# Performance work log

Hardware: AMD Instinct MI355X
Metric: run time of the kernel (lower is better)

Reference implementation:

```python
import jax, jax.numpy as jnp
import numpy as np

B, N, M = 4, 50000, 256
BIN_MIN, BIN_MAX = -3.0, 3.0


def setup_inputs() -> dict:
    key = jax.random.key(0)
    kx, ky = jax.random.split(key)
    x_coords = jax.random.normal(kx, (B, N), dtype=jnp.float32)
    y_coords = jax.random.normal(ky, (B, N), dtype=jnp.float32)
    bins = jnp.linspace(BIN_MIN, BIN_MAX, M, dtype=jnp.float32)
    return {"x_coords": x_coords, "y_coords": y_coords, "bins": bins}


def reference(x_coords, y_coords, bins):
    # bandwidth defaults to bin resolution (bins[1] - bins[0])
    bandwidth = bins[1] - bins[0]
    # per-axis Gaussian kernel values: (B, N, M)
    kx = jnp.exp(-0.5 * jnp.square((x_coords[..., None] - bins) / bandwidth))
    ky = jnp.exp(-0.5 * jnp.square((y_coords[..., None] - bins) / bandwidth))
    # joint kernel values reduced over particles: (B, M, M)
    joint = jnp.einsum("bni,bnj->bij", kx, ky)
    norm = jnp.sum(joint, axis=(-2, -1), keepdims=True) + 1e-10
    return joint / norm
```

## Files before the change

kernel.cpp:

```cpp
#include <hip/hip_runtime.h>


#define B_     4
#define N_     50000
#define M_     256
#define BK     64
#define NCH    48
#define KSTEPS 17
#define KCH    (KSTEPS * BK)
#define LDKB   80
#define ROWS   129
#define AXB    (ROWS * LDKB)
#define BUFB   (2 * AXB)
#define BLOCK  256
#define WINB   7
#define CS2    0.72134752f
#define L127   6.9886847f

#if __has_builtin(__builtin_amdgcn_exp2f)
  #define EXP2(t) __builtin_amdgcn_exp2f(t)
#else
  #define EXP2(t) exp2f(t)
#endif

typedef __attribute__((ext_vector_type(4))) int i32x4;

__device__ __forceinline__ unsigned short bf16ru(float f) {
    return (unsigned short)((__builtin_bit_cast(unsigned, f) + 0x8000u) >> 16);
}
__device__ __forceinline__ float bf2f(unsigned short u) {
    return __builtin_bit_cast(float, ((unsigned)u) << 16);
}

__global__ __launch_bounds__(BLOCK) void kde_gemm(
    const float* __restrict__ xs, const float* __restrict__ ys,
    const float* __restrict__ bins, unsigned short* __restrict__ partial,
    float* __restrict__ ws2, int wide)
{
    __shared__ __align__(16) char tiles[2][2][ROWS][LDKB];
    __shared__ float sred[4];

    const int tid   = threadIdx.x;
    const int tile  = blockIdx.x;
    const int chunk = blockIdx.y;
    const int b     = blockIdx.z;

    const int ilo = (tile & 1) * 128;
    const int jlo = (tile >> 1) * 128;
    const float bin0  = bins[0];
    const float invbw = 1.0f / (bins[1] - bin0);

    {
        int4* za = (int4*)&tiles[0][0][0][0];
        const int4 z4 = {0, 0, 0, 0};
        for (int t = tid; t < (int)(sizeof(tiles) / 16); t += BLOCK) za[t] = z4;
    }

    const int  h       = tid & 1;
    const int  jn      = 4 - h;
    const int  jbase   = h << 2;
    const int  kcol    = (tid >> 1) & 63;
    const int  axis    = (tid >> 7) & 1;
    const int  rowlo   = axis ? jlo : ilo;
    const int  colbase = axis * AXB + kcol;
    const float* coord = (axis ? ys : xs) + b * N_;
    const int  k0 = chunk * KCH;
    char* const tb = &tiles[0][0][0][0];

    const int w    = tid >> 6;
    const int R0   = (w >> 1) * 64;
    const int wj   = (w & 1) * 64;
    const int lane = tid & 63;
    const int lm   = lane & 15;
    const int quad = lane >> 4;
    unsigned short* pb = partial + (((size_t)chunk * B_ + b) << 16);

    i32x4 acc[4][4];
    #pragma unroll
    for (int mt = 0; mt < 4; ++mt)
        #pragma unroll
        for (int nt = 0; nt < 4; ++nt) acc[mt][nt] = i32x4{0, 0, 0, 0};

    int ps0 = 1 << 20, ps1 = 1 << 20;

    float v0 = 3.0e30f, vnext = 3.0e30f;
    {
        const int ka = k0 + kcol;       if (ka  < N_) v0    = coord[ka];
        const int kb2 = k0 + BK + kcol; if (kb2 < N_) vnext = coord[kb2];
    }
    __syncthreads();

    {
        const float u  = (v0 - bin0) * invbw;
        const float st = rintf(u) - 3.0f;
        const float d0 = u - st;
        const int rr0 = (int)st - rowlo;
        ps0 = rr0;
        const int dmp = colbase + 128 * LDKB;
        #pragma unroll
        for (int j = 0; j < 4; ++j) {
            if (j < jn) {
                const int jj = jbase + j;
                const float d = d0 - (float)jj;
                const float E = EXP2(fmaf(-CS2 * d, d, L127));
                const int rr = rr0 + jj;
                tb[((unsigned)rr < 128u) ? (colbase + rr * LDKB) : dmp] =
                    (char)(int)(E + 0.5f);
            }
        }
    }
    __syncthreads();

    for (int ks = 0; ks < KSTEPS; ++ks) {
        const int q = ks & 1;
        float vpre = 3.0e30f;
        if ((ks + 2) < KSTEPS) {
            const int ka = k0 + (ks + 2) * BK + kcol;
            if (ka < N_) vpre = coord[ka];
        }
        if ((ks + 1) < KSTEPS) {
            const int qn  = q ^ 1;
            const int bqn = qn * BUFB + colbase;
            const int dmp = bqn + 128 * LDKB;
            const int ps  = qn ? ps1 : ps0;
            if (ps < (1 << 19)) {
                #pragma unroll
                for (int j = 0; j < 4; ++j) {
                    if (j < jn) {
                        const int rr = ps + jbase + j;
                        tb[((unsigned)rr < 128u) ? (bqn + rr * LDKB) : dmp] = 0;
                    }
                }
            }
            const float u  = (vnext - bin0) * invbw;
            const float st = rintf(u) - 3.0f;
            const float d0 = u - st;
            const int rr0 = (int)st - rowlo;
            if (qn) ps1 = rr0; else ps0 = rr0;
            #pragma unroll
            for (int j = 0; j < 4; ++j) {
                if (j < jn) {
                    const int jj = jbase + j;
                    const float d = d0 - (float)jj;
                    const float E = EXP2(fmaf(-CS2 * d, d, L127));
                    const int rr = rr0 + jj;
                    tb[((unsigned)rr < 128u) ? (bqn + rr * LDKB) : dmp] =
                        (char)(int)(E + 0.5f);
                }
            }
        }
        vnext = vpre;

        const char* bufA = tb + q * BUFB;
        const char* bufB = tb + q * BUFB + AXB;
        i32x4 af[4], bfr[4];
        #pragma unroll
        for (int t4 = 0; t4 < 4; ++t4)
            af[t4] = *(const i32x4*)(bufA + (R0 + t4 * 16 + lm) * LDKB + quad * 16);
        #pragma unroll
        for (int t4 = 0; t4 < 4; ++t4)
            bfr[t4] = *(const i32x4*)(bufB + (wj + t4 * 16 + lm) * LDKB + quad * 16);
        #pragma unroll
        for (int mt = 0; mt < 4; ++mt)
            #pragma unroll
            for (int nt = 0; nt < 4; ++nt)
                acc[mt][nt] = __builtin_amdgcn_mfma_i32_16x16x64_i8(
                    af[mt], bfr[nt], acc[mt][nt], 0, 0, 0);
        __syncthreads();
    }

    float tsum = 0.f;
    #pragma unroll
    for (int mt = 0; mt < 4; ++mt) {
        const int row0 = ilo + R0 + mt * 16 + quad * 4;
        #pragma unroll
        for (int nt = 0; nt < 4; ++nt) {
            const int col = jlo + wj + nt * 16 + lm;
            const i32x4 a = acc[mt][nt];
            #pragma unroll
            for (int e = 0; e < 4; ++e) {
                const float v = (float)a[e];
                pb[(size_t)(row0 + e) * M_ + col] = bf16ru(v);
                tsum += v;
            }
        }
    }

    #pragma unroll
    for (int off = 32; off; off >>= 1) tsum += __shfl_xor(tsum, off);
    if (lane == 0) sred[w] = tsum;
    __syncthreads();
    if (tid == 0) {
        const float bsum = sred[0] + sred[1] + sred[2] + sred[3];
        if (wide) {
            const int bid = (b * NCH + chunk) * 4 + tile;
            ws2[bid] = bsum;
        } else {
            atomicAdd(&ws2[b], bsum);
        }
    }
}

__global__ __launch_bounds__(BLOCK) void kde_tail(
    const unsigned short* __restrict__ partial, const float* __restrict__ ws2,
    float* __restrict__ out, int wide)
{
    __shared__ float sred[4];
    __shared__ float snorm;
    const int tid = threadIdx.x;
    const int cellIdx = blockIdx.x * BLOCK + tid;
    const int bb = cellIdx >> 14;
    const int cb = cellIdx & 16383;

    float nrm;
    if (wide) {
        float t = (tid < 4 * NCH) ? ws2[bb * 4 * NCH + tid] : 0.f;
        #pragma unroll
        for (int off = 32; off; off >>= 1) t += __shfl_xor(t, off);
        if ((tid & 63) == 0) sred[tid >> 6] = t;
        __syncthreads();
        if (tid == 0) snorm = sred[0] + sred[1] + sred[2] + sred[3];
        __syncthreads();
        nrm = snorm;
    } else {
        nrm = ws2[bb];
    }

    float4 a = {0.f, 0.f, 0.f, 0.f};
    #pragma unroll 4
    for (int c = 0; c < NCH; ++c) {
        const ushort4 v = *(const ushort4*)(partial +
            (((size_t)c * B_ + bb) << 16) + (size_t)cb * 4);
        a.x += bf2f(v.x); a.y += bf2f(v.y); a.z += bf2f(v.z); a.w += bf2f(v.w);
    }
    const float sc = 1.0f / (nrm + 1e-10f);
    a.x *= sc; a.y *= sc; a.z *= sc; a.w *= sc;
    ((float4*)out)[cellIdx] = a;
}

extern "C" void kernel_launch(void* const* d_in, const int* in_sizes, int n_in,
                              void* d_out, int out_size, void* d_ws, size_t ws_size,
                              hipStream_t stream)
{
    const float* xs   = (const float*)d_in[0];
    const float* ys   = (const float*)d_in[1];
    const float* bins = (const float*)d_in[2];
    float* out = (float*)d_out;
    unsigned short* partial = (unsigned short*)d_ws;
    const size_t PSZ = (size_t)NCH * B_ * M_ * M_ * sizeof(unsigned short);
    float* ws2 = (float*)((char*)d_ws + PSZ);

    const int wide = (ws_size >= PSZ + 4096) ? 1 : 0;
    if (!wide) hipMemsetAsync(ws2, 0, 4 * sizeof(float), stream);

    kde_gemm<<<dim3(4, NCH, B_), dim3(BLOCK), 0, stream>>>(
        xs, ys, bins, partial, ws2, wide);
    kde_tail<<<dim3(B_ * M_ * M_ / (4 * BLOCK)), dim3(BLOCK), 0, stream>>>(
        partial, ws2, out, wide);
}
```

Baseline: 88.16 us.

## Pre-bucket particles per output tile so GEMM skips non-contributing particles

```diff
diff --git a/kernel.cpp b/kernel.cpp
--- a/kernel.cpp
+++ b/kernel.cpp
@@ -6,14 +6,12 @@
 #define M_     256
 #define BK     64
 #define NCH    48
-#define KSTEPS 17
-#define KCH    (KSTEPS * BK)
 #define LDKB   80
 #define ROWS   129
 #define AXB    (ROWS * LDKB)
 #define BUFB   (2 * AXB)
 #define BLOCK  256
-#define WINB   7
+#define CAP    65536
 #define CS2    0.72134752f
 #define L127   6.9886847f
 
@@ -32,10 +30,112 @@
     return __builtin_bit_cast(float, ((unsigned)u) << 16);
 }
 
+__global__ __launch_bounds__(BLOCK) void kde_bucket(
+    const float* __restrict__ xs, const float* __restrict__ ys,
+    const float* __restrict__ bins, int4* __restrict__ lists,
+    int* __restrict__ counts)
+{
+    const int b = blockIdx.y;
+    const int k = blockIdx.x * BLOCK + threadIdx.x;
+    const float bin0  = bins[0];
+    const float invbw = 1.0f / (bins[1] - bin0);
+    const bool valid = (k < N_);
+
+    const float x = valid ? xs[b * N_ + k] : 3.0e30f;
+    const float y = valid ? ys[b * N_ + k] : 3.0e30f;
+    const float ux = (x - bin0) * invbw;
+    const float uy = (y - bin0) * invbw;
+    const float stx = rintf(ux) - 3.0f;
+    const float sty = rintf(uy) - 3.0f;
+    const float dx0 = ux - stx;
+    const float dy0 = uy - sty;
+    const int rx = (int)stx;
+    const int ry = (int)sty;
+
+    unsigned qx[7], qy[7];
+    #pragma unroll
+    for (int j = 0; j < 7; ++j) {
+        const float dx = dx0 - (float)j;
+        const float dy = dy0 - (float)j;
+        qx[j] = (unsigned)(int)(EXP2(fmaf(-CS2 * dx, dx, L127)) + 0.5f) & 255u;
+        qy[j] = (unsigned)(int)(EXP2(fmaf(-CS2 * dy, dy, L127)) + 0.5f) & 255u;
+    }
+
+    const bool mx[2] = { valid && rx >= -6  && rx <= 127,
+                         valid && rx >= 122 && rx <= 255 };
+    const bool my[2] = { valid && ry >= -6  && ry <= 127,
+                         valid && ry >= 122 && ry <= 255 };
+
+    const int lane = threadIdx.x & 63;
+    #pragma unroll
+    for (int ti = 0; ti < 2; ++ti) {
+        #pragma unroll
+        for (int tj = 0; tj < 2; ++tj) {
+            const bool m = mx[ti] && my[tj];
+            const unsigned long long mask = __ballot(m);
+            if (mask) {
+                const int li = (b * 2 + ti) * 2 + tj;
+                const int leader = __ffsll((unsigned long long)mask) - 1;
+                int base = 0;
+                if (lane == leader)
+                    base = atomicAdd(&counts[li], __popcll(mask));
+                base = __shfl(base, leader);
+                if (m) {
+                    const int off =
+                        __popcll(mask & ((1ull << lane) - 1ull));
+                    const unsigned rxl = (unsigned)(rx - ti * 128 + 8) & 255u;
+                    const unsigned ryl = (unsigned)(ry - tj * 128 + 8) & 255u;
+                    int4 e;
+                    e.x = (int)(rxl | (ryl << 8) | (qx[0] << 16) | (qx[1] << 24));
+                    e.y = (int)(qx[2] | (qx[3] << 8) | (qx[4] << 16) | (qx[5] << 24));
+                    e.z = (int)(qx[6] | (qy[0] << 8) | (qy[1] << 16) | (qy[2] << 24));
+                    e.w = (int)(qy[3] | (qy[4] << 8) | (qy[5] << 16) | (qy[6] << 24));
+                    lists[(size_t)li * CAP + base + off] = e;
+                }
+            }
+        }
+    }
+}
+
+__device__ __forceinline__ void scat(char* __restrict__ tb, const int4 e,
+                                     const int axis, const int h,
+                                     const int cbq, int& ps)
+{
+    const int jbase = h << 2;
+    const int dmp = cbq + 128 * LDKB;
+    if (ps < (1 << 19)) {
+        const int pr = ps + jbase;
+        tb[((unsigned)(pr    ) < 128u) ? (cbq + (pr    ) * LDKB) : dmp] = 0;
+        tb[((unsigned)(pr + 1) < 128u) ? (cbq + (pr + 1) * LDKB) : dmp] = 0;
+        tb[((unsigned)(pr + 2) < 128u) ? (cbq + (pr + 2) * LDKB) : dmp] = 0;
+        if (!h)
+            tb[((unsigned)(pr + 3) < 128u) ? (cbq + (pr + 3) * LDKB) : dmp] = 0;
+    }
+    const int rl = ((axis ? (e.x >> 8) : e.x) & 255) - 8;
+    int q0, q1, q2, q3;
+    if (axis == 0) {
+        q0 = h ? ((e.y >> 16) & 255) : ((e.x >> 16) & 255);
+        q1 = h ? (int)((unsigned)e.y >> 24) : (int)((unsigned)e.x >> 24);
+        q2 = h ? (e.z & 255) : (e.y & 255);
+        q3 = (e.y >> 8) & 255;
+    } else {
+        q0 = h ? ((e.w >> 8) & 255) : ((e.z >> 8) & 255);
+        q1 = h ? ((e.w >> 16) & 255) : ((e.z >> 16) & 255);
+        q2 = h ? (int)((unsigned)e.w >> 24) : (int)((unsigned)e.z >> 24);
+        q3 = e.w & 255;
+    }
+    ps = rl;
+    const int rr = rl + jbase;
+    tb[((unsigned)(rr    ) < 128u) ? (cbq + (rr    ) * LDKB) : dmp] = (char)q0;
+    tb[((unsigned)(rr + 1) < 128u) ? (cbq + (rr + 1) * LDKB) : dmp] = (char)q1;
+    tb[((unsigned)(rr + 2) < 128u) ? (cbq + (rr + 2) * LDKB) : dmp] = (char)q2;
+    if (!h)
+        tb[((unsigned)(rr + 3) < 128u) ? (cbq + (rr + 3) * LDKB) : dmp] = (char)q3;
+}
+
 __global__ __launch_bounds__(BLOCK) void kde_gemm(
-    const float* __restrict__ xs, const float* __restrict__ ys,
-    const float* __restrict__ bins, unsigned short* __restrict__ partial,
-    float* __restrict__ ws2, int wide)
+    const int4* __restrict__ lists, const int* __restrict__ counts,
+    unsigned short* __restrict__ partial, float* __restrict__ ws2, int wide)
 {
     __shared__ __align__(16) char tiles[2][2][ROWS][LDKB];
     __shared__ float sred[4];
@@ -45,10 +145,20 @@
     const int chunk = blockIdx.y;
     const int b     = blockIdx.z;
 
-    const int ilo = (tile & 1) * 128;
-    const int jlo = (tile >> 1) * 128;
-    const float bin0  = bins[0];
-    const float invbw = 1.0f / (bins[1] - bin0);
+    const int ti  = tile & 1;
+    const int tj  = tile >> 1;
+    const int ilo = ti * 128;
+    const int jlo = tj * 128;
+
+    const int li  = (b * 2 + ti) * 2 + tj;
+    const int len = counts[li];
+    const int seg = (len + NCH - 1) / NCH;
+    const int start = chunk * seg;
+    int myn = len - start;
+    if (myn < 0) myn = 0;
+    if (myn > seg) myn = seg;
+    const int ksteps = (myn + 63) >> 6;
+    const int4* lst = lists + (size_t)li * CAP + start;
 
     {
         int4* za = (int4*)&tiles[0][0][0][0];
@@ -56,15 +166,10 @@
         for (int t = tid; t < (int)(sizeof(tiles) / 16); t += BLOCK) za[t] = z4;
     }
 
-    const int  h       = tid & 1;
-    const int  jn      = 4 - h;
-    const int  jbase   = h << 2;
-    const int  kcol    = (tid >> 1) & 63;
-    const int  axis    = (tid >> 7) & 1;
-    const int  rowlo   = axis ? jlo : ilo;
-    const int  colbase = axis * AXB + kcol;
-    const float* coord = (axis ? ys : xs) + b * N_;
-    const int  k0 = chunk * KCH;
+    const int h     = tid & 1;
+    const int kcol  = (tid >> 1) & 63;
+    const int axis  = (tid >> 7) & 1;
+    const int colbase = axis * AXB + kcol;
     char* const tb = &tiles[0][0][0][0];
 
     const int w    = tid >> 6;
@@ -83,73 +188,27 @@
 
     int ps0 = 1 << 20, ps1 = 1 << 20;
 
-    float v0 = 3.0e30f, vnext = 3.0e30f;
-    {
-        const int ka = k0 + kcol;       if (ka  < N_) v0    = coord[ka];
-        const int kb2 = k0 + BK + kcol; if (kb2 < N_) vnext = coord[kb2];
-    }
+    const int4 DUM = {0x0000FFFF, 0, 0, 0};
+    int4 e0 = DUM, enext = DUM;
+    if (kcol < myn)      e0    = lst[kcol];
+    if (BK + kcol < myn) enext = lst[BK + kcol];
+
     __syncthreads();
 
-    {
-        const float u  = (v0 - bin0) * invbw;
-        const float st = rintf(u) - 3.0f;
-        const float d0 = u - st;
-        const int rr0 = (int)st - rowlo;
-        ps0 = rr0;
-        const int dmp = colbase + 128 * LDKB;
-        #pragma unroll
-        for (int j = 0; j < 4; ++j) {
-            if (j < jn) {
-                const int jj = jbase + j;
-                const float d = d0 - (float)jj;
-                const float E = EXP2(fmaf(-CS2 * d, d, L127));
-                const int rr = rr0 + jj;
-                tb[((unsigned)rr < 128u) ? (colbase + rr * LDKB) : dmp] =
-                    (char)(int)(E + 0.5f);
-            }
+    if (ksteps > 0)
+        scat(tb, e0, axis, h, colbase, ps0);
+    __syncthreads();
+
+    for (int ks = 0; ks < ksteps; ++ks) {
+        const int q = ks & 1;
+        int4 epre = DUM;
+        const int ka = (ks + 2) * BK + kcol;
+        if ((ks + 2) < ksteps && ka < myn) epre = lst[ka];
+        if ((ks + 1) < ksteps) {
+            if (q) scat(tb, enext, axis, h, colbase, ps0);
+            else   scat(tb, enext, axis, h, BUFB + colbase, ps1);
         }
-    }
-    __syncthreads();
-
-    for (int ks = 0; ks < KSTEPS; ++ks) {
-        const int q = ks & 1;
-        float vpre = 3.0e30f;
-        if ((ks + 2) < KSTEPS) {
-            const int ka = k0 + (ks + 2) * BK + kcol;
-            if (ka < N_) vpre = coord[ka];
-        }
-        if ((ks + 1) < KSTEPS) {
-            const int qn  = q ^ 1;
-            const int bqn = qn * BUFB + colbase;
-            const int dmp = bqn + 128 * LDKB;
-            const int ps  = qn ? ps1 : ps0;
-            if (ps < (1 << 19)) {
-                #pragma unroll
-                for (int j = 0; j < 4; ++j) {
-                    if (j < jn) {
-                        const int rr = ps + jbase + j;
-                        tb[((unsigned)rr < 128u) ? (bqn + rr * LDKB) : dmp] = 0;
-                    }
-                }
-            }
-            const float u  = (vnext - bin0) * invbw;
-            const float st = rintf(u) - 3.0f;
-            const float d0 = u - st;
-            const int rr0 = (int)st - rowlo;
-            if (qn) ps1 = rr0; else ps0 = rr0;
-            #pragma unroll
-            for (int j = 0; j < 4; ++j) {
-                if (j < jn) {
-                    const int jj = jbase + j;
-                    const float d = d0 - (float)jj;
-                    const float E = EXP2(fmaf(-CS2 * d, d, L127));
-                    const int rr = rr0 + jj;
-                    tb[((unsigned)rr < 128u) ? (bqn + rr * LDKB) : dmp] =
-                        (char)(int)(E + 0.5f);
-                }
-            }
-        }
-        vnext = vpre;
+        enext = epre;
 
         const char* bufA = tb + q * BUFB;
         const char* bufB = tb + q * BUFB + AXB;
@@ -246,15 +305,21 @@
     const float* ys   = (const float*)d_in[1];
     const float* bins = (const float*)d_in[2];
     float* out = (float*)d_out;
+
     unsigned short* partial = (unsigned short*)d_ws;
     const size_t PSZ = (size_t)NCH * B_ * M_ * M_ * sizeof(unsigned short);
-    float* ws2 = (float*)((char*)d_ws + PSZ);
+    float* ws2   = (float*)((char*)d_ws + PSZ);
+    int*   counts = (int*)((char*)d_ws + PSZ + 4096);
+    int4*  lists  = (int4*)((char*)d_ws + PSZ + 8192);
 
     const int wide = (ws_size >= PSZ + 4096) ? 1 : 0;
     if (!wide) hipMemsetAsync(ws2, 0, 4 * sizeof(float), stream);
-
+    hipMemsetAsync(counts, 0, 16 * sizeof(int), stream);
+
+    kde_bucket<<<dim3((N_ + BLOCK - 1) / BLOCK, B_), dim3(BLOCK), 0, stream>>>(
+        xs, ys, bins, lists, counts);
     kde_gemm<<<dim3(4, NCH, B_), dim3(BLOCK), 0, stream>>>(
-        xs, ys, bins, partial, ws2, wide);
+        lists, counts, partial, ws2, wide);
     kde_tail<<<dim3(B_ * M_ * M_ / (4 * BLOCK)), dim3(BLOCK), 0, stream>>>(
         partial, ws2, out, wide);
 }
```

Measured after the change: 226.2 us. +156.6%, slower.

## Replace int8 MFMA outer-product GEMM with LDS atomic scatter of 7x7 stencils

Applied to the files above, without the earlier changes.

```diff
diff --git a/kernel.cpp b/kernel.cpp
--- a/kernel.cpp
+++ b/kernel.cpp
@@ -4,16 +4,13 @@
 #define B_     4
 #define N_     50000
 #define M_     256
-#define BK     64
-#define NCH    48
-#define KSTEPS 17
-#define KCH    (KSTEPS * BK)
-#define LDKB   80
-#define ROWS   129
-#define AXB    (ROWS * LDKB)
-#define BUFB   (2 * AXB)
+#define NCH    32
+#define NST    2
+#define CHUNK  ((N_ + NCH - 1) / NCH)
 #define BLOCK  256
-#define WINB   7
+#define GROWS  128
+#define GCELLS (GROWS * M_)
+#define GSZ    33088
 #define CS2    0.72134752f
 #define L127   6.9886847f
 
@@ -23,8 +20,6 @@
   #define EXP2(t) exp2f(t)
 #endif
 
-typedef __attribute__((ext_vector_type(4))) int i32x4;
-
 __device__ __forceinline__ unsigned short bf16ru(float f) {
     return (unsigned short)((__builtin_bit_cast(unsigned, f) + 0x8000u) >> 16);
 }
@@ -32,158 +27,98 @@
     return __builtin_bit_cast(float, ((unsigned)u) << 16);
 }
 
-__global__ __launch_bounds__(BLOCK) void kde_gemm(
+__global__ __launch_bounds__(BLOCK) void kde_accum(
     const float* __restrict__ xs, const float* __restrict__ ys,
     const float* __restrict__ bins, unsigned short* __restrict__ partial,
     float* __restrict__ ws2, int wide)
 {
-    __shared__ __align__(16) char tiles[2][2][ROWS][LDKB];
+    __shared__ __align__(16) unsigned int G[GSZ];
     __shared__ float sred[4];
 
     const int tid   = threadIdx.x;
-    const int tile  = blockIdx.x;
+    const int strip = blockIdx.x;
     const int chunk = blockIdx.y;
     const int b     = blockIdx.z;
+    const int lane  = tid & 63;
+    const int w     = tid >> 6;
 
-    const int ilo = (tile & 1) * 128;
-    const int jlo = (tile >> 1) * 128;
     const float bin0  = bins[0];
     const float invbw = 1.0f / (bins[1] - bin0);
+    const int   rlo   = strip * GROWS;
 
     {
-        int4* za = (int4*)&tiles[0][0][0][0];
-        const int4 z4 = {0, 0, 0, 0};
-        for (int t = tid; t < (int)(sizeof(tiles) / 16); t += BLOCK) za[t] = z4;
-    }
-
-    const int  h       = tid & 1;
-    const int  jn      = 4 - h;
-    const int  jbase   = h << 2;
-    const int  kcol    = (tid >> 1) & 63;
-    const int  axis    = (tid >> 7) & 1;
-    const int  rowlo   = axis ? jlo : ilo;
-    const int  colbase = axis * AXB + kcol;
-    const float* coord = (axis ? ys : xs) + b * N_;
-    const int  k0 = chunk * KCH;
-    char* const tb = &tiles[0][0][0][0];
-
-    const int w    = tid >> 6;
-    const int R0   = (w >> 1) * 64;
-    const int wj   = (w & 1) * 64;
-    const int lane = tid & 63;
-    const int lm   = lane & 15;
-    const int quad = lane >> 4;
-    unsigned short* pb = partial + (((size_t)chunk * B_ + b) << 16);
-
-    i32x4 acc[4][4];
-    #pragma unroll
-    for (int mt = 0; mt < 4; ++mt)
-        #pragma unroll
-        for (int nt = 0; nt < 4; ++nt) acc[mt][nt] = i32x4{0, 0, 0, 0};
-
-    int ps0 = 1 << 20, ps1 = 1 << 20;
-
-    float v0 = 3.0e30f, vnext = 3.0e30f;
-    {
-        const int ka = k0 + kcol;       if (ka  < N_) v0    = coord[ka];
-        const int kb2 = k0 + BK + kcol; if (kb2 < N_) vnext = coord[kb2];
+        uint4* gz = (uint4*)G;
+        const uint4 z4 = {0u, 0u, 0u, 0u};
+        for (int t = tid; t < GSZ / 4; t += BLOCK) gz[t] = z4;
     }
     __syncthreads();
 
-    {
-        const float u  = (v0 - bin0) * invbw;
-        const float st = rintf(u) - 3.0f;
-        const float d0 = u - st;
-        const int rr0 = (int)st - rowlo;
-        ps0 = rr0;
-        const int dmp = colbase + 128 * LDKB;
-        #pragma unroll
-        for (int j = 0; j < 4; ++j) {
-            if (j < jn) {
-                const int jj = jbase + j;
-                const float d = d0 - (float)jj;
-                const float E = EXP2(fmaf(-CS2 * d, d, L127));
-                const int rr = rr0 + jj;
-                tb[((unsigned)rr < 128u) ? (colbase + rr * LDKB) : dmp] =
-                    (char)(int)(E + 0.5f);
+    const int start = chunk * CHUNK;
+    const int end   = (start + CHUNK < N_) ? (start + CHUNK) : N_;
+    const float* xp = xs + (size_t)b * N_;
+    const float* yp = ys + (size_t)b * N_;
+
+    const unsigned dmp = (unsigned)(GCELLS + lane);
+
+    int k = start + tid;
+    float x = 3.0e30f, y = 3.0e30f;
+    if (k < end) { x = xp[k]; y = yp[k]; }
+    for (; k < end; k += BLOCK) {
+        float xn = 3.0e30f, yn = 3.0e30f;
+        if (k + BLOCK < end) { xn = xp[k + BLOCK]; yn = yp[k + BLOCK]; }
+
+        const float ux  = (x - bin0) * invbw;
+        const float uy  = (y - bin0) * invbw;
+        const float stx = rintf(ux) - 3.0f;
+        const float sty = rintf(uy) - 3.0f;
+        const int rx = (int)stx;
+        const int ry = (int)sty;
+
+        if (rx + 6 >= rlo && rx < rlo + GROWS && ry + 6 >= 0 && ry < M_) {
+            const float dx0 = ux - stx;
+            const float dy0 = uy - sty;
+            unsigned qx[7], qy[7], cofs[7];
+            #pragma unroll
+            for (int j = 0; j < 7; ++j) {
+                const float dx = dx0 - (float)j;
+                const float dy = dy0 - (float)j;
+                qx[j] = (unsigned)(int)(EXP2(fmaf(-CS2 * dx, dx, L127)) + 0.5f);
+                qy[j] = (unsigned)(int)(EXP2(fmaf(-CS2 * dy, dy, L127)) + 0.5f);
+                const int c = ry + j;
+                cofs[j] = ((unsigned)c < (unsigned)M_) ? (unsigned)c : 0x80000000u;
+            }
+            #pragma unroll
+            for (int i = 0; i < 7; ++i) {
+                const int rr = rx + i - rlo;
+                const unsigned rbase =
+                    ((unsigned)rr < (unsigned)GROWS) ? (unsigned)(rr << 8) : dmp;
+                const unsigned wxi = qx[i];
+                #pragma unroll
+                for (int j = 0; j < 7; ++j) {
+                    unsigned addr = rbase + cofs[j];
+                    addr = ((int)addr < 0) ? dmp : addr;
+                    atomicAdd(&G[addr], wxi * qy[j]);
+                }
             }
         }
+        x = xn; y = yn;
     }
     __syncthreads();
 
-    for (int ks = 0; ks < KSTEPS; ++ks) {
-        const int q = ks & 1;
-        float vpre = 3.0e30f;
-        if ((ks + 2) < KSTEPS) {
-            const int ka = k0 + (ks + 2) * BK + kcol;
-            if (ka < N_) vpre = coord[ka];
-        }
-        if ((ks + 1) < KSTEPS) {
-            const int qn  = q ^ 1;
-            const int bqn = qn * BUFB + colbase;
-            const int dmp = bqn + 128 * LDKB;
-            const int ps  = qn ? ps1 : ps0;
-            if (ps < (1 << 19)) {
-                #pragma unroll
-                for (int j = 0; j < 4; ++j) {
-                    if (j < jn) {
-                        const int rr = ps + jbase + j;
-                        tb[((unsigned)rr < 128u) ? (bqn + rr * LDKB) : dmp] = 0;
-                    }
-                }
-            }
-            const float u  = (vnext - bin0) * invbw;
-            const float st = rintf(u) - 3.0f;
-            const float d0 = u - st;
-            const int rr0 = (int)st - rowlo;
-            if (qn) ps1 = rr0; else ps0 = rr0;
-            #pragma unroll
-            for (int j = 0; j < 4; ++j) {
-                if (j < jn) {
-                    const int jj = jbase + j;
-                    const float d = d0 - (float)jj;
-                    const float E = EXP2(fmaf(-CS2 * d, d, L127));
-                    const int rr = rr0 + jj;
-                    tb[((unsigned)rr < 128u) ? (bqn + rr * LDKB) : dmp] =
-                        (char)(int)(E + 0.5f);
-                }
-            }
-        }
-        vnext = vpre;
-
-        const char* bufA = tb + q * BUFB;
-        const char* bufB = tb + q * BUFB + AXB;
-        i32x4 af[4], bfr[4];
-        #pragma unroll
-        for (int t4 = 0; t4 < 4; ++t4)
-            af[t4] = *(const i32x4*)(bufA + (R0 + t4 * 16 + lm) * LDKB + quad * 16);
-        #pragma unroll
-        for (int t4 = 0; t4 < 4; ++t4)
-            bfr[t4] = *(const i32x4*)(bufB + (wj + t4 * 16 + lm) * LDKB + quad * 16);
-        #pragma unroll
-        for (int mt = 0; mt < 4; ++mt)
-            #pragma unroll
-            for (int nt = 0; nt < 4; ++nt)
-                acc[mt][nt] = __builtin_amdgcn_mfma_i32_16x16x64_i8(
-                    af[mt], bfr[nt], acc[mt][nt], 0, 0, 0);
-        __syncthreads();
-    }
-
+    unsigned short* pb = partial + (((size_t)chunk * B_ + b) << 16);
     float tsum = 0.f;
     #pragma unroll
-    for (int mt = 0; mt < 4; ++mt) {
-        const int row0 = ilo + R0 + mt * 16 + quad * 4;
-        #pragma unroll
-        for (int nt = 0; nt < 4; ++nt) {
-            const int col = jlo + wj + nt * 16 + lm;
-            const i32x4 a = acc[mt][nt];
-            #pragma unroll
-            for (int e = 0; e < 4; ++e) {
-                const float v = (float)a[e];
-                pb[(size_t)(row0 + e) * M_ + col] = bf16ru(v);
-                tsum += v;
-            }
-        }
+    for (int rep = 0; rep < GCELLS / (BLOCK * 4); ++rep) {
+        const int cell = rep * (BLOCK * 4) + tid * 4;
+        const uint4 gv = *(const uint4*)&G[cell];
+        const float f0 = (float)gv.x, f1 = (float)gv.y;
+        const float f2 = (float)gv.z, f3 = (float)gv.w;
+        tsum += (f0 + f1) + (f2 + f3);
+        ushort4 o;
+        o.x = bf16ru(f0); o.y = bf16ru(f1); o.z = bf16ru(f2); o.w = bf16ru(f3);
+        const int r = cell >> 8;
+        const int c = cell & (M_ - 1);
+        *(ushort4*)&pb[(size_t)(rlo + r) * M_ + c] = o;
     }
 
     #pragma unroll
@@ -193,7 +128,7 @@
     if (tid == 0) {
         const float bsum = sred[0] + sred[1] + sred[2] + sred[3];
         if (wide) {
-            const int bid = (b * NCH + chunk) * 4 + tile;
+            const int bid = (b * NCH + chunk) * NST + strip;
             ws2[bid] = bsum;
         } else {
             atomicAdd(&ws2[b], bsum);
@@ -214,7 +149,7 @@
 
     float nrm;
     if (wide) {
-        float t = (tid < 4 * NCH) ? ws2[bb * 4 * NCH + tid] : 0.f;
+        float t = (tid < NCH * NST) ? ws2[bb * (NCH * NST) + tid] : 0.f;
         #pragma unroll
         for (int off = 32; off; off >>= 1) t += __shfl_xor(t, off);
         if ((tid & 63) == 0) sred[tid >> 6] = t;
@@ -246,6 +181,7 @@
     const float* ys   = (const float*)d_in[1];
     const float* bins = (const float*)d_in[2];
     float* out = (float*)d_out;
+
     unsigned short* partial = (unsigned short*)d_ws;
     const size_t PSZ = (size_t)NCH * B_ * M_ * M_ * sizeof(unsigned short);
     float* ws2 = (float*)((char*)d_ws + PSZ);
@@ -253,7 +189,7 @@
     const int wide = (ws_size >= PSZ + 4096) ? 1 : 0;
     if (!wide) hipMemsetAsync(ws2, 0, 4 * sizeof(float), stream);
 
-    kde_gemm<<<dim3(4, NCH, B_), dim3(BLOCK), 0, stream>>>(
+    kde_accum<<<dim3(NST, NCH, B_), dim3(BLOCK), 0, stream>>>(
         xs, ys, bins, partial, ws2, wide);
     kde_tail<<<dim3(B_ * M_ * M_ / (4 * BLOCK)), dim3(BLOCK), 0, stream>>>(
         partial, ws2, out, wide);
```

Result: faster. 81.63 us (-7.4%).
